# Performance work log

Measured on AMD Instinct MI355X. Metric: run time of the kernel, lower is better.

Reference implementation:

```python
import jax, jax.numpy as jnp
import numpy as np

D_MODEL = 768
MIMO_RANK = 4


def setup_inputs() -> dict:
    key = jax.random.key(0)
    ks = jax.random.split(key, 6)
    B, T, D, R = 2, 2048, D_MODEL, MIMO_RANK
    x = jax.random.normal(ks[0], (B, T, D), dtype=jnp.float32)
    norm_w = jnp.ones((D,), dtype=jnp.float32)
    W_in = jax.random.normal(ks[1], (D * R * 2, D), dtype=jnp.float32) * 0.02
    W_out = jax.random.normal(ks[2], (D, D), dtype=jnp.float32) * 0.02
    a_param = jax.random.normal(ks[3], (D, R, 2), dtype=jnp.float32) * 0.12
    b_param = jax.random.normal(ks[4], (D, R, 2), dtype=jnp.float32) * 0.15
    c_param = jax.random.normal(ks[5], (D, R, 2), dtype=jnp.float32) * 0.15
    return {"x": x, "norm_w": norm_w, "W_in": W_in, "W_out": W_out,
            "a_param": a_param, "b_param": b_param, "c_param": c_param}


def reference(x, norm_w, W_in, W_out, a_param, b_param, c_param):
    B, T, D = x.shape
    R = a_param.shape[1]
    # RMSNorm
    xn = x * jax.lax.rsqrt(jnp.mean(x * x, axis=-1, keepdims=True) + 1e-6) * norm_w
    # in_proj -> interleaved complex MIMO input u: [B,T,D,R,2]
    u = (xn @ W_in.T).reshape(B, T, D, R, 2)
    # coefficients (tanh-bounded; |a| scaled by 0.97 for stability)
    a = jnp.tanh(a_param) * 0.97
    b = jnp.tanh(b_param)
    c = jnp.tanh(c_param)
    ac = jax.lax.complex(a[..., 0], a[..., 1])  # [D,R]
    bc = jax.lax.complex(b[..., 0], b[..., 1])
    cc = jax.lax.complex(c[..., 0], c[..., 1])
    uc = jax.lax.complex(u[..., 0], u[..., 1])  # [B,T,D,R]
    # linear complex recurrence s_t = a * s_{t-1} + b * u_t, zero init state,
    # parallelized with an associative scan over time.
    bu = bc[None, None] * uc
    A = jnp.broadcast_to(ac[None, None], bu.shape)

    def comb(l, r):
        return (l[0] * r[0], r[0] * l[1] + r[1])

    _, s = jax.lax.associative_scan(comb, (A, bu), axis=1)  # [B,T,D,R] complex
    # output mix: real part of c * h, summed over MIMO rank -> [B,T,D]
    y = jnp.real(cc[None, None] * s).sum(axis=-1)
    return y @ W_out.T
```

## Files before the change

### kernel.cpp

```cpp
#include <hip/hip_runtime.h>
#include <hip/hip_bf16.h>
#include <stdint.h>

#define BATCH 2
#define TT 2048
#define DM 768
#define RR 4
#define M_TOK 4096
#define NFEAT 6144
#define NCH 6144
#define CHUNK 64
#define NCHUNK 32

typedef __attribute__((ext_vector_type(8))) short short8;
typedef __attribute__((ext_vector_type(4))) float float4v;

__device__ inline float bf2f(uint32_t bits16) {
    union { uint32_t u; float f; } x; x.u = bits16 << 16; return x.f;
}

typedef const __attribute__((address_space(1))) void* gptr_t;
typedef __attribute__((address_space(3))) void* lptr_t;

__device__ inline void async_ld16(const void* g, void* l) {
    __builtin_amdgcn_global_load_lds((gptr_t)(uintptr_t)g, (lptr_t)(uintptr_t)l,
                                     16, 0, 0);
}

__device__ inline void store_c(__hip_bfloat16* C, size_t idx, float v) {
    C[idx] = __float2bfloat16(v);
}
__device__ inline void store_c(float* C, size_t idx, float v) { C[idx] = v; }

__device__ inline uint2 pack4bf(float a, float b, float c, float d) {
    union { __hip_bfloat16 h[4]; uint2 u; } o;
    o.h[0] = __float2bfloat16(a); o.h[1] = __float2bfloat16(b);
    o.h[2] = __float2bfloat16(c); o.h[3] = __float2bfloat16(d);
    return o.u;
}

__device__ inline float2 cmul(float2 a, float2 b) {
    return make_float2(a.x * b.x - a.y * b.y, a.x * b.y + a.y * b.x);
}

__device__ inline void cstep(float& sr, float& si, float2 a, float2 bb,
                             uint32_t uw) {
    float ur = bf2f(uw & 0xffffu), ui = bf2f(uw >> 16);
    float tr = bb.x * ur - bb.y * ui;
    float ti = bb.x * ui + bb.y * ur;
    float nr = a.x * sr - a.y * si + tr;
    float ni = a.x * si + a.y * sr + ti;
    sr = nr; si = ni;
}

__global__ __launch_bounds__(256) void prep_rms(
    const float* __restrict__ x, const float* __restrict__ w,
    const float* __restrict__ W_in, const float* __restrict__ W_out,
    const float* __restrict__ ap, const float* __restrict__ bp,
    const float* __restrict__ cp,
    __hip_bfloat16* __restrict__ xn,
    __hip_bfloat16* __restrict__ Win_bf, __hip_bfloat16* __restrict__ Wout_bf,
    float2* __restrict__ ac, float2* __restrict__ bc,
    float2* __restrict__ cc, float2* __restrict__ aL) {
    int bid = blockIdx.x;
    int tid = threadIdx.x;
    if (bid < M_TOK) {
        __shared__ float wsum[3];
        float4 v = make_float4(0.f, 0.f, 0.f, 0.f);
        if (tid < 192) v = ((const float4*)(x + (size_t)bid * DM))[tid];
        float ss = v.x * v.x + v.y * v.y + v.z * v.z + v.w * v.w;
        #pragma unroll
        for (int o = 1; o < 64; o <<= 1) ss += __shfl_xor(ss, o);
        if (tid < 192 && (tid & 63) == 0) wsum[tid >> 6] = ss;
        __syncthreads();
        if (tid < 192) {
            float tot = wsum[0] + wsum[1] + wsum[2];
            float scale = rsqrtf(tot * (1.f / DM) + 1e-6f);
            float4 wv = ((const float4*)w)[tid];
            ((uint2*)(xn + (size_t)bid * DM))[tid] =
                pack4bf(v.x * scale * wv.x, v.y * scale * wv.y,
                        v.z * scale * wv.z, v.w * scale * wv.w);
        }
        return;
    }
    const int N1 = NFEAT * DM / 4;
    const int N2 = DM * DM / 4;
    int i = (bid - M_TOK) * 256 + tid;
    if (i < N1) {
        float4 v = ((const float4*)W_in)[i];
        ((uint2*)Win_bf)[i] = pack4bf(v.x, v.y, v.z, v.w);
    } else if (i < N1 + N2) {
        int k = i - N1;
        float4 v = ((const float4*)W_out)[k];
        ((uint2*)Wout_bf)[k] = pack4bf(v.x, v.y, v.z, v.w);
    }
    if (i < DM * RR) {
        float ar = tanhf(ap[2 * i])     * 0.97f;
        float ai = tanhf(ap[2 * i + 1]) * 0.97f;
        ac[i] = make_float2(ar, ai);
        bc[i] = make_float2(tanhf(bp[2 * i]), tanhf(bp[2 * i + 1]));
        cc[i] = make_float2(tanhf(cp[2 * i]), tanhf(cp[2 * i + 1]));
        float xr = ar, xi = ai;
        #pragma unroll
        for (int k = 0; k < 6; ++k) {
            float nr = xr * xr - xi * xi;
            float ni = 2.f * xr * xi;
            xr = nr; xi = ni;
        }
        aL[i] = make_float2(xr, xi);
    }
}

template <int BM, int BN, int BK, typename OutT>
__device__ inline void gemm_body(
    const __hip_bfloat16* __restrict__ A, const __hip_bfloat16* __restrict__ B,
    OutT* __restrict__ C, int K, int ldc) {
    constexpr int MI = BM / 32;
    constexpr int NJ = BN / 32;
    constexpr int CPR = BK / 8;
    __shared__ __attribute__((aligned(16))) __hip_bfloat16 lA[BM * BK];
    __shared__ __attribute__((aligned(16))) __hip_bfloat16 lB[BN * BK];
    const int tid  = threadIdx.x;
    const int lane = tid & 63;
    const int wave = tid >> 6;
    const int quad = lane >> 4;
    const int l15  = lane & 15;
    const int wm = (wave >> 1) * (BM / 2);
    const int wn = (wave & 1) * (BN / 2);
    const int m0 = blockIdx.y * BM;
    const int n0 = blockIdx.x * BN;

    float4v acc[MI][NJ] = {};

    for (int k0 = 0; k0 < K; k0 += BK) {
        __syncthreads();
        #pragma unroll
        for (int it = 0; it < BM * CPR / 256; ++it) {
            int p = it * 256 + tid;
            int row = p / CPR;
            int cg = (p & (CPR - 1)) ^ (row & (CPR - 1));
            async_ld16(A + (size_t)(m0 + row) * K + k0 + cg * 8, lA + p * 8);
        }
        #pragma unroll
        for (int it = 0; it < BN * CPR / 256; ++it) {
            int p = it * 256 + tid;
            int row = p / CPR;
            int cg = (p & (CPR - 1)) ^ (row & (CPR - 1));
            async_ld16(B + (size_t)(n0 + row) * K + k0 + cg * 8, lB + p * 8);
        }
        __syncthreads();
        #pragma unroll
        for (int s = 0; s < BK / 32; ++s) {
            short8 af[MI], bfr[NJ];
            #pragma unroll
            for (int i = 0; i < MI; ++i) {
                int r = wm + i * 16 + l15;
                int c = (s * 4 + quad) ^ (r & (CPR - 1));
                af[i] = *(const short8*)(lA + r * BK + c * 8);
            }
            #pragma unroll
            for (int j = 0; j < NJ; ++j) {
                int r = wn + j * 16 + l15;
                int c = (s * 4 + quad) ^ (r & (CPR - 1));
                bfr[j] = *(const short8*)(lB + r * BK + c * 8);
            }
            #pragma unroll
            for (int i = 0; i < MI; ++i)
                #pragma unroll
                for (int j = 0; j < NJ; ++j)
                    acc[i][j] = __builtin_amdgcn_mfma_f32_16x16x32_bf16(
                        af[i], bfr[j], acc[i][j], 0, 0, 0);
        }
    }
    #pragma unroll
    for (int i = 0; i < MI; ++i)
        #pragma unroll
        for (int j = 0; j < NJ; ++j)
            #pragma unroll
            for (int rg = 0; rg < 4; ++rg) {
                int row = m0 + wm + i * 16 + quad * 4 + rg;
                int col = n0 + wn + j * 16 + l15;
                store_c(C, (size_t)row * ldc + col, acc[i][j][rg]);
            }
}

__global__ __launch_bounds__(256) void gemm_in(
    const __hip_bfloat16* __restrict__ A, const __hip_bfloat16* __restrict__ B,
    __hip_bfloat16* __restrict__ C, int K) {
    gemm_body<128, 128, 64, __hip_bfloat16>(A, B, C, K, NFEAT);
}

__global__ __launch_bounds__(256) void gemm_out(
    const __hip_bfloat16* __restrict__ A, const __hip_bfloat16* __restrict__ B,
    float* __restrict__ C, int K) {
    gemm_body<64, 64, 128, float>(A, B, C, K, DM);
}

__global__ __launch_bounds__(256) void scan_local(
    const uint4* __restrict__ u4,
    const float2* __restrict__ ac, const float2* __restrict__ bc,
    const float2* __restrict__ cc,
    __hip_bfloat16* __restrict__ y_local,
    float2* __restrict__ chunkEnd) {
    int g = blockIdx.x * 256 + threadIdx.x;
    int j = blockIdx.y;
    int b = g >= DM;
    int d = g - b * DM;
    int cb = d * RR;
    float2 a0 = ac[cb], a1 = ac[cb + 1], a2 = ac[cb + 2], a3 = ac[cb + 3];
    float2 b0 = bc[cb], b1 = bc[cb + 1], b2 = bc[cb + 2], b3 = bc[cb + 3];
    float2 c0 = cc[cb], c1 = cc[cb + 1], c2 = cc[cb + 2], c3 = cc[cb + 3];
    float s0r = 0, s0i = 0, s1r = 0, s1i = 0;
    float s2r = 0, s2i = 0, s3r = 0, s3i = 0;
    size_t base = ((size_t)(b * TT + j * CHUNK)) * DM + d;
    #pragma unroll 4
    for (int i = 0; i < CHUNK; ++i) {
        uint4 uw = u4[base + (size_t)i * DM];
        cstep(s0r, s0i, a0, b0, uw.x);
        cstep(s1r, s1i, a1, b1, uw.y);
        cstep(s2r, s2i, a2, b2, uw.z);
        cstep(s3r, s3i, a3, b3, uw.w);
        float yv = c0.x * s0r - c0.y * s0i + c1.x * s1r - c1.y * s1i
                 + c2.x * s2r - c2.y * s2i + c3.x * s3r - c3.y * s3i;
        y_local[base + (size_t)i * DM] = __float2bfloat16(yv);
    }
    size_t eb = (size_t)j * NCH + b * (DM * RR) + cb;
    chunkEnd[eb]     = make_float2(s0r, s0i);
    chunkEnd[eb + 1] = make_float2(s1r, s1i);
    chunkEnd[eb + 2] = make_float2(s2r, s2i);
    chunkEnd[eb + 3] = make_float2(s3r, s3i);
}

__global__ __launch_bounds__(256) void scan_fix(
    const __hip_bfloat16* __restrict__ y_local,
    const float2* __restrict__ ac, const float2* __restrict__ cc,
    const float2* __restrict__ aLp, const float2* __restrict__ chunkEnd,
    __hip_bfloat16* __restrict__ y) {
    int g = blockIdx.x * 256 + threadIdx.x;
    int j = blockIdx.y;
    int b = g >= DM;
    int d = g - b * DM;
    int cb = d * RR;
    float2 a0 = ac[cb], a1 = ac[cb + 1], a2 = ac[cb + 2], a3 = ac[cb + 3];
    float2 aL0 = aLp[cb], aL1 = aLp[cb + 1], aL2 = aLp[cb + 2], aL3 = aLp[cb + 3];
    float2 k0 = make_float2(0, 0), k1 = k0, k2 = k0, k3 = k0;
    for (int jj = 0; jj < j; ++jj) {
        size_t eb = (size_t)jj * NCH + b * (DM * RR) + cb;
        float2 e0 = chunkEnd[eb],     e1 = chunkEnd[eb + 1];
        float2 e2 = chunkEnd[eb + 2], e3 = chunkEnd[eb + 3];
        float nr, ni;
        nr = aL0.x * k0.x - aL0.y * k0.y + e0.x; ni = aL0.x * k0.y + aL0.y * k0.x + e0.y; k0 = make_float2(nr, ni);
        nr = aL1.x * k1.x - aL1.y * k1.y + e1.x; ni = aL1.x * k1.y + aL1.y * k1.x + e1.y; k1 = make_float2(nr, ni);
        nr = aL2.x * k2.x - aL2.y * k2.y + e2.x; ni = aL2.x * k2.y + aL2.y * k2.x + e2.y; k2 = make_float2(nr, ni);
        nr = aL3.x * k3.x - aL3.y * k3.y + e3.x; ni = aL3.x * k3.y + aL3.y * k3.x + e3.y; k3 = make_float2(nr, ni);
    }
    float2 q0 = cmul(cmul(cc[cb],     k0), a0);
    float2 q1 = cmul(cmul(cc[cb + 1], k1), a1);
    float2 q2 = cmul(cmul(cc[cb + 2], k2), a2);
    float2 q3 = cmul(cmul(cc[cb + 3], k3), a3);
    size_t base = ((size_t)(b * TT + j * CHUNK)) * DM + d;
    #pragma unroll 4
    for (int i = 0; i < CHUNK; ++i) {
        float yv = bf2f(((const uint16_t*)y_local)[base + (size_t)i * DM])
                 + q0.x + q1.x + q2.x + q3.x;
        y[base + (size_t)i * DM] = __float2bfloat16(yv);
        q0 = cmul(q0, a0); q1 = cmul(q1, a1);
        q2 = cmul(q2, a2); q3 = cmul(q3, a3);
    }
}

extern "C" void kernel_launch(void* const* d_in, const int* in_sizes, int n_in,
                              void* d_out, int out_size, void* d_ws,
                              size_t ws_size, hipStream_t stream) {
    const float* x      = (const float*)d_in[0];
    const float* norm_w = (const float*)d_in[1];
    const float* W_in   = (const float*)d_in[2];
    const float* W_out  = (const float*)d_in[3];
    const float* a_p    = (const float*)d_in[4];
    const float* b_p    = (const float*)d_in[5];
    const float* c_p    = (const float*)d_in[6];
    float* out = (float*)d_out;

    char* ws = (char*)d_ws;
    size_t off = 0;
    auto alloc = [&](size_t bytes) {
        void* p = ws + off;
        off += (bytes + 255) & ~(size_t)255;
        return p;
    };
    __hip_bfloat16* Win_bf  = (__hip_bfloat16*)alloc((size_t)NFEAT * DM * 2);
    __hip_bfloat16* Wout_bf = (__hip_bfloat16*)alloc((size_t)DM * DM * 2);
    __hip_bfloat16* xn      = (__hip_bfloat16*)alloc((size_t)M_TOK * DM * 2);
    __hip_bfloat16* u       = (__hip_bfloat16*)alloc((size_t)M_TOK * NFEAT * 2);
    __hip_bfloat16* y_local = (__hip_bfloat16*)alloc((size_t)M_TOK * DM * 2);
    __hip_bfloat16* y       = (__hip_bfloat16*)alloc((size_t)M_TOK * DM * 2);
    float2* ac = (float2*)alloc((size_t)DM * RR * 8);
    float2* bc = (float2*)alloc((size_t)DM * RR * 8);
    float2* cc = (float2*)alloc((size_t)DM * RR * 8);
    float2* aL = (float2*)alloc((size_t)DM * RR * 8);
    float2* chunkEnd = (float2*)alloc((size_t)NCHUNK * NCH * 8);

    {
        int cast_blocks = ((NFEAT * DM + DM * DM) / 4 + 255) / 256;
        prep_rms<<<M_TOK + cast_blocks, 256, 0, stream>>>(
            x, norm_w, W_in, W_out, a_p, b_p, c_p,
            xn, Win_bf, Wout_bf, ac, bc, cc, aL);
    }
    gemm_in<<<dim3(NFEAT / 128, M_TOK / 128), 256, 0, stream>>>(
        xn, Win_bf, u, DM);
    scan_local<<<dim3(BATCH * DM / 256, NCHUNK), 256, 0, stream>>>(
        (const uint4*)u, ac, bc, cc, y_local, chunkEnd);
    scan_fix<<<dim3(BATCH * DM / 256, NCHUNK), 256, 0, stream>>>(
        y_local, ac, cc, aL, chunkEnd, y);
    gemm_out<<<dim3(DM / 64, M_TOK / 64), 256, 0, stream>>>(
        y, Wout_bf, out, DM);
}
```

Measured before the change: 192.8 us.

## Fuse in-projection GEMM with chunk-local complex scan via LDS epilogue

The in-projection GEMM and the chunk-local scan are merged into one kernel. Each 128x128 output tile is packed to bf16 in shared memory, and 128 threads then run the per-chunk recurrence directly from LDS, using shuffles to reduce over the rank. This removes the write and re-read of the large u intermediate (about 50 MB of bf16) in global memory. In exchange, half the block sits idle during a serial 64-step scan epilogue, which lengthens the GEMM kernel's tail.

Result: slower. 199.5 us (+3.5%).

```diff
diff --git a/kernel.cpp b/kernel.cpp
--- a/kernel.cpp
+++ b/kernel.cpp
@@ -36,6 +36,12 @@
     union { __hip_bfloat16 h[4]; uint2 u; } o;
     o.h[0] = __float2bfloat16(a); o.h[1] = __float2bfloat16(b);
     o.h[2] = __float2bfloat16(c); o.h[3] = __float2bfloat16(d);
+    return o.u;
+}
+
+__device__ inline uint32_t pack2bf(float a, float b) {
+    union { __hip_bfloat16 h[2]; uint32_t u; } o;
+    o.h[0] = __float2bfloat16(a); o.h[1] = __float2bfloat16(b);
     return o.u;
 }
 
@@ -184,51 +190,128 @@
             }
 }
 
-__global__ __launch_bounds__(256) void gemm_in(
-    const __hip_bfloat16* __restrict__ A, const __hip_bfloat16* __restrict__ B,
-    __hip_bfloat16* __restrict__ C, int K) {
-    gemm_body<128, 128, 64, __hip_bfloat16>(A, B, C, K, NFEAT);
-}
-
 __global__ __launch_bounds__(256) void gemm_out(
     const __hip_bfloat16* __restrict__ A, const __hip_bfloat16* __restrict__ B,
     float* __restrict__ C, int K) {
     gemm_body<64, 64, 128, float>(A, B, C, K, DM);
 }
 
-__global__ __launch_bounds__(256) void scan_local(
-    const uint4* __restrict__ u4,
+__global__ __launch_bounds__(256) void gemm_in_scan(
+    const __hip_bfloat16* __restrict__ A,
+    const __hip_bfloat16* __restrict__ B,
     const float2* __restrict__ ac, const float2* __restrict__ bc,
     const float2* __restrict__ cc,
     __hip_bfloat16* __restrict__ y_local,
     float2* __restrict__ chunkEnd) {
-    int g = blockIdx.x * 256 + threadIdx.x;
-    int j = blockIdx.y;
-    int b = g >= DM;
-    int d = g - b * DM;
-    int cb = d * RR;
-    float2 a0 = ac[cb], a1 = ac[cb + 1], a2 = ac[cb + 2], a3 = ac[cb + 3];
-    float2 b0 = bc[cb], b1 = bc[cb + 1], b2 = bc[cb + 2], b3 = bc[cb + 3];
-    float2 c0 = cc[cb], c1 = cc[cb + 1], c2 = cc[cb + 2], c3 = cc[cb + 3];
-    float s0r = 0, s0i = 0, s1r = 0, s1i = 0;
-    float s2r = 0, s2i = 0, s3r = 0, s3i = 0;
-    size_t base = ((size_t)(b * TT + j * CHUNK)) * DM + d;
-    #pragma unroll 4
-    for (int i = 0; i < CHUNK; ++i) {
-        uint4 uw = u4[base + (size_t)i * DM];
-        cstep(s0r, s0i, a0, b0, uw.x);
-        cstep(s1r, s1i, a1, b1, uw.y);
-        cstep(s2r, s2i, a2, b2, uw.z);
-        cstep(s3r, s3i, a3, b3, uw.w);
-        float yv = c0.x * s0r - c0.y * s0i + c1.x * s1r - c1.y * s1i
-                 + c2.x * s2r - c2.y * s2i + c3.x * s3r - c3.y * s3i;
-        y_local[base + (size_t)i * DM] = __float2bfloat16(yv);
-    }
-    size_t eb = (size_t)j * NCH + b * (DM * RR) + cb;
-    chunkEnd[eb]     = make_float2(s0r, s0i);
-    chunkEnd[eb + 1] = make_float2(s1r, s1i);
-    chunkEnd[eb + 2] = make_float2(s2r, s2i);
-    chunkEnd[eb + 3] = make_float2(s3r, s3i);
+    constexpr int BM = 128, BN = 128, BK = 64;
+    constexpr int MI = BM / 32, NJ = BN / 32, CPR = BK / 8;
+    constexpr int K = DM;
+    __shared__ __attribute__((aligned(16))) __hip_bfloat16 smem[BM * BK + BN * BK];
+    __hip_bfloat16* lA = smem;
+    __hip_bfloat16* lB = smem + BM * BK;
+    const int tid  = threadIdx.x;
+    const int lane = tid & 63;
+    const int wave = tid >> 6;
+    const int quad = lane >> 4;
+    const int l15  = lane & 15;
+    const int wm = (wave >> 1) * (BM / 2);
+    const int wn = (wave & 1) * (BN / 2);
+    const int m0 = blockIdx.y * BM;
+    const int n0 = blockIdx.x * BN;
+
+    float4v acc[MI][NJ] = {};
+
+    for (int k0 = 0; k0 < K; k0 += BK) {
+        __syncthreads();
+        #pragma unroll
+        for (int it = 0; it < BM * CPR / 256; ++it) {
+            int p = it * 256 + tid;
+            int row = p / CPR;
+            int cg = (p & (CPR - 1)) ^ (row & (CPR - 1));
+            async_ld16(A + (size_t)(m0 + row) * K + k0 + cg * 8, lA + p * 8);
+        }
+        #pragma unroll
+        for (int it = 0; it < BN * CPR / 256; ++it) {
+            int p = it * 256 + tid;
+            int row = p / CPR;
+            int cg = (p & (CPR - 1)) ^ (row & (CPR - 1));
+            async_ld16(B + (size_t)(n0 + row) * K + k0 + cg * 8, lB + p * 8);
+        }
+        __syncthreads();
+        #pragma unroll
+        for (int s = 0; s < BK / 32; ++s) {
+            short8 af[MI], bfr[NJ];
+            #pragma unroll
+            for (int i = 0; i < MI; ++i) {
+                int r = wm + i * 16 + l15;
+                int c = (s * 4 + quad) ^ (r & (CPR - 1));
+                af[i] = *(const short8*)(lA + r * BK + c * 8);
+            }
+            #pragma unroll
+            for (int j = 0; j < NJ; ++j) {
+                int r = wn + j * 16 + l15;
+                int c = (s * 4 + quad) ^ (r & (CPR - 1));
+                bfr[j] = *(const short8*)(lB + r * BK + c * 8);
+            }
+            #pragma unroll
+            for (int i = 0; i < MI; ++i)
+                #pragma unroll
+                for (int j = 0; j < NJ; ++j)
+                    acc[i][j] = __builtin_amdgcn_mfma_f32_16x16x32_bf16(
+                        af[i], bfr[j], acc[i][j], 0, 0, 0);
+        }
+    }
+
+    __syncthreads();
+    uint32_t* up = (uint32_t*)smem;
+    #pragma unroll
+    for (int i = 0; i < MI; ++i)
+        #pragma unroll
+        for (int j = 0; j < NJ; ++j) {
+            float s0 = __shfl_xor(acc[i][j][0], 1);
+            float s1 = __shfl_xor(acc[i][j][1], 1);
+            float s2 = __shfl_xor(acc[i][j][2], 1);
+            float s3 = __shfl_xor(acc[i][j][3], 1);
+            const bool odd = l15 & 1;
+            float lo0 = odd ? s2 : acc[i][j][0];
+            float hi0 = odd ? acc[i][j][2] : s0;
+            float lo1 = odd ? s3 : acc[i][j][1];
+            float hi1 = odd ? acc[i][j][3] : s1;
+            int row0 = wm + i * 16 + quad * 4 + (odd ? 2 : 0);
+            int row1 = row0 + 1;
+            int pr = (wn + j * 16 + (l15 & ~1)) >> 1;
+            up[row0 * 64 + (pr ^ (row0 & 31))] = pack2bf(lo0, hi0);
+            up[row1 * 64 + (pr ^ (row1 & 31))] = pack2bf(lo1, hi1);
+        }
+    __syncthreads();
+
+    if (tid < 128) {
+        const int r     = tid & 3;
+        const int d_loc = (tid >> 2) & 15;
+        const int half  = tid >> 6;
+        const int d_g   = (n0 >> 3) + d_loc;
+        const int cb    = d_g * RR + r;
+        const float2 av = ac[cb];
+        const float2 bv = bc[cb];
+        const float2 cv = cc[cb];
+        const int bb = m0 >> 11;
+        const int j  = ((m0 & (TT - 1)) >> 6) + half;
+        const int p  = d_loc * 4 + r;
+        float sr = 0.f, si = 0.f;
+        size_t ybase = (size_t)(m0 + half * 64) * DM + d_g;
+        #pragma unroll 4
+        for (int t = 0; t < CHUNK; ++t) {
+            int row = half * 64 + t;
+            uint32_t uw = up[row * 64 + (p ^ (row & 31))];
+            cstep(sr, si, av, bv, uw);
+            float yv = cv.x * sr - cv.y * si;
+            yv += __shfl_xor(yv, 1);
+            yv += __shfl_xor(yv, 2);
+            if (r == 0)
+                y_local[ybase + (size_t)t * DM] = __float2bfloat16(yv);
+        }
+        chunkEnd[(size_t)j * NCH + bb * (DM * RR) + cb] = make_float2(sr, si);
+    }
 }
 
 __global__ __launch_bounds__(256) void scan_fix(
@@ -291,7 +374,6 @@
     __hip_bfloat16* Win_bf  = (__hip_bfloat16*)alloc((size_t)NFEAT * DM * 2);
     __hip_bfloat16* Wout_bf = (__hip_bfloat16*)alloc((size_t)DM * DM * 2);
     __hip_bfloat16* xn      = (__hip_bfloat16*)alloc((size_t)M_TOK * DM * 2);
-    __hip_bfloat16* u       = (__hip_bfloat16*)alloc((size_t)M_TOK * NFEAT * 2);
     __hip_bfloat16* y_local = (__hip_bfloat16*)alloc((size_t)M_TOK * DM * 2);
     __hip_bfloat16* y       = (__hip_bfloat16*)alloc((size_t)M_TOK * DM * 2);
     float2* ac = (float2*)alloc((size_t)DM * RR * 8);
@@ -306,10 +388,8 @@
             x, norm_w, W_in, W_out, a_p, b_p, c_p,
             xn, Win_bf, Wout_bf, ac, bc, cc, aL);
     }
-    gemm_in<<<dim3(NFEAT / 128, M_TOK / 128), 256, 0, stream>>>(
-        xn, Win_bf, u, DM);
-    scan_local<<<dim3(BATCH * DM / 256, NCHUNK), 256, 0, stream>>>(
-        (const uint4*)u, ac, bc, cc, y_local, chunkEnd);
+    gemm_in_scan<<<dim3(NFEAT / 128, M_TOK / 128), 256, 0, stream>>>(
+        xn, Win_bf, ac, bc, cc, y_local, chunkEnd);
     scan_fix<<<dim3(BATCH * DM / 256, NCHUNK), 256, 0, stream>>>(
         y_local, ac, cc, aL, chunkEnd, y);
     gemm_out<<<dim3(DM / 64, M_TOK / 64), 256, 0, stream>>>(
```

## Parallelize chunk scans with intra-block sub-chunk scan and split fix-up over time

Applied to the files above, without the earlier changes.

The local scan kernel now splits each 64-step chunk into eight 8-step sub-chunks handled by different threads. Each thread's sub-chunk end state goes into shared memory, and a short serial carry pass combines them inside the block, raising parallelism from 192 blocks to 1536. The fix-up kernel gains a third grid dimension so each 64-token chunk is corrected in four 16-token slices, using a precomputed a^16 power to jump the carry forward. This adds redundant carry work per thread and a block barrier, in exchange for far more in-flight threads on what was a latency-bound serial recurrence.

Result: faster. 175.8 us (-8.8%).

```diff
diff --git a/kernel.cpp b/kernel.cpp
--- a/kernel.cpp
+++ b/kernel.cpp
@@ -42,6 +42,13 @@
 __device__ inline float2 cmul(float2 a, float2 b) {
     return make_float2(a.x * b.x - a.y * b.y, a.x * b.y + a.y * b.x);
 }
+__device__ inline float2 cmad(float2 a, float2 b, float2 c) {
+    return make_float2(a.x * b.x - a.y * b.y + c.x,
+                       a.x * b.y + a.y * b.x + c.y);
+}
+__device__ inline float2 csq(float2 a) {
+    return make_float2(a.x * a.x - a.y * a.y, 2.f * a.x * a.y);
+}
 
 __device__ inline void cstep(float& sr, float& si, float2 a, float2 bb,
                              uint32_t uw) {
@@ -61,7 +68,8 @@
     __hip_bfloat16* __restrict__ xn,
     __hip_bfloat16* __restrict__ Win_bf, __hip_bfloat16* __restrict__ Wout_bf,
     float2* __restrict__ ac, float2* __restrict__ bc,
-    float2* __restrict__ cc, float2* __restrict__ aL) {
+    float2* __restrict__ cc, float2* __restrict__ aQ,
+    float2* __restrict__ aL) {
     int bid = blockIdx.x;
     int tid = threadIdx.x;
     if (bid < M_TOK) {
@@ -102,7 +110,14 @@
         cc[i] = make_float2(tanhf(cp[2 * i]), tanhf(cp[2 * i + 1]));
         float xr = ar, xi = ai;
         #pragma unroll
-        for (int k = 0; k < 6; ++k) {
+        for (int k = 0; k < 4; ++k) {
+            float nr = xr * xr - xi * xi;
+            float ni = 2.f * xr * xi;
+            xr = nr; xi = ni;
+        }
+        aQ[i] = make_float2(xr, xi);
+        #pragma unroll
+        for (int k = 0; k < 2; ++k) {
             float nr = xr * xr - xi * xi;
             float ni = 2.f * xr * xi;
             xr = nr; xi = ni;
@@ -196,48 +211,90 @@
     gemm_body<64, 64, 128, float>(A, B, C, K, DM);
 }
 
-__global__ __launch_bounds__(256) void scan_local(
+__global__ __launch_bounds__(256) void scan_local2(
     const uint4* __restrict__ u4,
     const float2* __restrict__ ac, const float2* __restrict__ bc,
     const float2* __restrict__ cc,
     __hip_bfloat16* __restrict__ y_local,
     float2* __restrict__ chunkEnd) {
-    int g = blockIdx.x * 256 + threadIdx.x;
-    int j = blockIdx.y;
-    int b = g >= DM;
-    int d = g - b * DM;
-    int cb = d * RR;
+    __shared__ float2 se[1024];
+    const int tid   = threadIdx.x;
+    const int d_loc = tid & 31;
+    const int s8    = tid >> 5;
+    const int bd    = blockIdx.x;
+    const int b     = bd >= 24;
+    const int dg    = bd - b * 24;
+    const int d_g   = dg * 32 + d_loc;
+    const int cb    = d_g * RR;
+    const int j     = blockIdx.y;
+
     float2 a0 = ac[cb], a1 = ac[cb + 1], a2 = ac[cb + 2], a3 = ac[cb + 3];
     float2 b0 = bc[cb], b1 = bc[cb + 1], b2 = bc[cb + 2], b3 = bc[cb + 3];
     float2 c0 = cc[cb], c1 = cc[cb + 1], c2 = cc[cb + 2], c3 = cc[cb + 3];
+
+    const int token0 = b * TT + j * CHUNK + s8 * 8;
+    const size_t base = (size_t)token0 * DM + d_g;
+
+    uint4 uw[8];
+    #pragma unroll
+    for (int i = 0; i < 8; ++i) uw[i] = u4[base + (size_t)i * DM];
     float s0r = 0, s0i = 0, s1r = 0, s1i = 0;
     float s2r = 0, s2i = 0, s3r = 0, s3i = 0;
-    size_t base = ((size_t)(b * TT + j * CHUNK)) * DM + d;
-    #pragma unroll 4
-    for (int i = 0; i < CHUNK; ++i) {
-        uint4 uw = u4[base + (size_t)i * DM];
-        cstep(s0r, s0i, a0, b0, uw.x);
-        cstep(s1r, s1i, a1, b1, uw.y);
-        cstep(s2r, s2i, a2, b2, uw.z);
-        cstep(s3r, s3i, a3, b3, uw.w);
-        float yv = c0.x * s0r - c0.y * s0i + c1.x * s1r - c1.y * s1i
-                 + c2.x * s2r - c2.y * s2i + c3.x * s3r - c3.y * s3i;
+    float yloc[8];
+    #pragma unroll
+    for (int i = 0; i < 8; ++i) {
+        cstep(s0r, s0i, a0, b0, uw[i].x);
+        cstep(s1r, s1i, a1, b1, uw[i].y);
+        cstep(s2r, s2i, a2, b2, uw[i].z);
+        cstep(s3r, s3i, a3, b3, uw[i].w);
+        yloc[i] = c0.x * s0r - c0.y * s0i + c1.x * s1r - c1.y * s1i
+                + c2.x * s2r - c2.y * s2i + c3.x * s3r - c3.y * s3i;
+    }
+    se[tid * 4]     = make_float2(s0r, s0i);
+    se[tid * 4 + 1] = make_float2(s1r, s1i);
+    se[tid * 4 + 2] = make_float2(s2r, s2i);
+    se[tid * 4 + 3] = make_float2(s3r, s3i);
+    __syncthreads();
+
+    float2 aE0 = csq(csq(csq(a0))), aE1 = csq(csq(csq(a1)));
+    float2 aE2 = csq(csq(csq(a2))), aE3 = csq(csq(csq(a3)));
+    float2 C0 = make_float2(0, 0), C1 = C0, C2 = C0, C3 = C0;
+    for (int k = 0; k < s8; ++k) {
+        int kb = (k * 32 + d_loc) * 4;
+        C0 = cmad(C0, aE0, se[kb]);
+        C1 = cmad(C1, aE1, se[kb + 1]);
+        C2 = cmad(C2, aE2, se[kb + 2]);
+        C3 = cmad(C3, aE3, se[kb + 3]);
+    }
+    if (s8 == 7) {
+        size_t eb = (size_t)j * NCH + b * (DM * RR) + cb;
+        chunkEnd[eb]     = cmad(C0, aE0, make_float2(s0r, s0i));
+        chunkEnd[eb + 1] = cmad(C1, aE1, make_float2(s1r, s1i));
+        chunkEnd[eb + 2] = cmad(C2, aE2, make_float2(s2r, s2i));
+        chunkEnd[eb + 3] = cmad(C3, aE3, make_float2(s3r, s3i));
+    }
+    float2 q0 = cmul(cmul(c0, C0), a0);
+    float2 q1 = cmul(cmul(c1, C1), a1);
+    float2 q2 = cmul(cmul(c2, C2), a2);
+    float2 q3 = cmul(cmul(c3, C3), a3);
+    #pragma unroll
+    for (int i = 0; i < 8; ++i) {
+        float yv = yloc[i] + q0.x + q1.x + q2.x + q3.x;
         y_local[base + (size_t)i * DM] = __float2bfloat16(yv);
-    }
-    size_t eb = (size_t)j * NCH + b * (DM * RR) + cb;
-    chunkEnd[eb]     = make_float2(s0r, s0i);
-    chunkEnd[eb + 1] = make_float2(s1r, s1i);
-    chunkEnd[eb + 2] = make_float2(s2r, s2i);
-    chunkEnd[eb + 3] = make_float2(s3r, s3i);
+        q0 = cmul(q0, a0); q1 = cmul(q1, a1);
+        q2 = cmul(q2, a2); q3 = cmul(q3, a3);
+    }
 }
 
 __global__ __launch_bounds__(256) void scan_fix(
     const __hip_bfloat16* __restrict__ y_local,
     const float2* __restrict__ ac, const float2* __restrict__ cc,
-    const float2* __restrict__ aLp, const float2* __restrict__ chunkEnd,
+    const float2* __restrict__ aQp, const float2* __restrict__ aLp,
+    const float2* __restrict__ chunkEnd,
     __hip_bfloat16* __restrict__ y) {
     int g = blockIdx.x * 256 + threadIdx.x;
     int j = blockIdx.y;
+    int z = blockIdx.z;
     int b = g >= DM;
     int d = g - b * DM;
     int cb = d * RR;
@@ -248,19 +305,21 @@
         size_t eb = (size_t)jj * NCH + b * (DM * RR) + cb;
         float2 e0 = chunkEnd[eb],     e1 = chunkEnd[eb + 1];
         float2 e2 = chunkEnd[eb + 2], e3 = chunkEnd[eb + 3];
-        float nr, ni;
-        nr = aL0.x * k0.x - aL0.y * k0.y + e0.x; ni = aL0.x * k0.y + aL0.y * k0.x + e0.y; k0 = make_float2(nr, ni);
-        nr = aL1.x * k1.x - aL1.y * k1.y + e1.x; ni = aL1.x * k1.y + aL1.y * k1.x + e1.y; k1 = make_float2(nr, ni);
-        nr = aL2.x * k2.x - aL2.y * k2.y + e2.x; ni = aL2.x * k2.y + aL2.y * k2.x + e2.y; k2 = make_float2(nr, ni);
-        nr = aL3.x * k3.x - aL3.y * k3.y + e3.x; ni = aL3.x * k3.y + aL3.y * k3.x + e3.y; k3 = make_float2(nr, ni);
+        k0 = cmad(k0, aL0, e0); k1 = cmad(k1, aL1, e1);
+        k2 = cmad(k2, aL2, e2); k3 = cmad(k3, aL3, e3);
     }
     float2 q0 = cmul(cmul(cc[cb],     k0), a0);
     float2 q1 = cmul(cmul(cc[cb + 1], k1), a1);
     float2 q2 = cmul(cmul(cc[cb + 2], k2), a2);
     float2 q3 = cmul(cmul(cc[cb + 3], k3), a3);
-    size_t base = ((size_t)(b * TT + j * CHUNK)) * DM + d;
+    float2 aQ0 = aQp[cb], aQ1 = aQp[cb + 1], aQ2 = aQp[cb + 2], aQ3 = aQp[cb + 3];
+    for (int zz = 0; zz < z; ++zz) {
+        q0 = cmul(q0, aQ0); q1 = cmul(q1, aQ1);
+        q2 = cmul(q2, aQ2); q3 = cmul(q3, aQ3);
+    }
+    size_t base = ((size_t)(b * TT + j * CHUNK + z * 16)) * DM + d;
     #pragma unroll 4
-    for (int i = 0; i < CHUNK; ++i) {
+    for (int i = 0; i < 16; ++i) {
         float yv = bf2f(((const uint16_t*)y_local)[base + (size_t)i * DM])
                  + q0.x + q1.x + q2.x + q3.x;
         y[base + (size_t)i * DM] = __float2bfloat16(yv);
@@ -297,6 +356,7 @@
     float2* ac = (float2*)alloc((size_t)DM * RR * 8);
     float2* bc = (float2*)alloc((size_t)DM * RR * 8);
     float2* cc = (float2*)alloc((size_t)DM * RR * 8);
+    float2* aQ = (float2*)alloc((size_t)DM * RR * 8);
     float2* aL = (float2*)alloc((size_t)DM * RR * 8);
     float2* chunkEnd = (float2*)alloc((size_t)NCHUNK * NCH * 8);
 
@@ -304,14 +364,14 @@
         int cast_blocks = ((NFEAT * DM + DM * DM) / 4 + 255) / 256;
         prep_rms<<<M_TOK + cast_blocks, 256, 0, stream>>>(
             x, norm_w, W_in, W_out, a_p, b_p, c_p,
-            xn, Win_bf, Wout_bf, ac, bc, cc, aL);
+            xn, Win_bf, Wout_bf, ac, bc, cc, aQ, aL);
     }
     gemm_in<<<dim3(NFEAT / 128, M_TOK / 128), 256, 0, stream>>>(
         xn, Win_bf, u, DM);
-    scan_local<<<dim3(BATCH * DM / 256, NCHUNK), 256, 0, stream>>>(
+    scan_local2<<<dim3(48, NCHUNK), 256, 0, stream>>>(
         (const uint4*)u, ac, bc, cc, y_local, chunkEnd);
-    scan_fix<<<dim3(BATCH * DM / 256, NCHUNK), 256, 0, stream>>>(
-        y_local, ac, cc, aL, chunkEnd, y);
+    scan_fix<<<dim3(BATCH * DM / 256, NCHUNK, 4), 256, 0, stream>>>(
+        y_local, ac, cc, aQ, aL, chunkEnd, y);
     gemm_out<<<dim3(DM / 64, M_TOK / 64), 256, 0, stream>>>(
         y, Wout_bf, out, DM);
 }
```
